# Performance work log

Hardware: AMD Instinct MI355X
Metric: run time of the kernel (lower is better)

Reference implementation:

```python
import jax, jax.numpy as jnp
from jax import lax
import numpy as np

B, C, H, W = 16, 32, 128, 128
R = 8      # region_num
OUT = 32   # out_channels (== in_channels, required by residual add)
K = 3      # kernel_size
PAD = 1    # self.kwargs padding for the correlation conv


def setup_inputs() -> dict:
    key = jax.random.key(0)
    ks = jax.random.split(key, 8)
    n = lambda k, s: jax.random.normal(k, s, dtype=jnp.float32) * 0.05
    return {
        "input": jax.random.normal(ks[0], (B, C, H, W), dtype=jnp.float32),
        "guide_input": jax.random.normal(ks[1], (B, C, H, W), dtype=jnp.float32),
        "w1": n(ks[2], (R * R, C)), "b1": jnp.zeros((R * R,), jnp.float32),
        "w2": n(ks[3], (R, C * OUT, R)), "b2": jnp.zeros((R * C * OUT,), jnp.float32),
        "w_spa": n(ks[4], (R, C)), "b_spa": jnp.zeros((R,), jnp.float32),
        "w_spec": n(ks[5], (R, C)), "b_spec": jnp.zeros((R,), jnp.float32),
        "w_f": n(ks[6], (OUT, 2 * C, 3, 3)), "b_f": jnp.zeros((OUT,), jnp.float32),
    }


def adaptive_avg_pool2d(x, k):
    # torch AdaptiveAvgPool2d bin edges: start=floor(i*H/k), end=ceil((i+1)*H/k)
    Hh, Ww = x.shape[-2], x.shape[-1]
    rows = []
    for i in range(k):
        hs, he = (i * Hh) // k, -(-((i + 1) * Hh) // k)
        cols = []
        for j in range(k):
            ws, we = (j * Ww) // k, -(-((j + 1) * Ww) // k)
            cols.append(x[..., hs:he, ws:we].mean(axis=(-2, -1)))
        rows.append(jnp.stack(cols, axis=-1))
    return jnp.stack(rows, axis=-2)  # [..., k, k]


def asign_index(kernel, guide):
    # kernel: [B, R, OUT, H, W]; guide: [B, R, H, W]
    mask = jax.nn.one_hot(jnp.argmax(guide, axis=1), guide.shape[1], axis=1,
                          dtype=kernel.dtype)  # [B, R, H, W]
    return jnp.sum(kernel * mask[:, :, None], axis=1)  # [B, OUT, H, W]


def reference(input, guide_input, w1, b1, w2, b2, w_spa, b_spa, w_spec, b_spec, w_f, b_f):
    # --- dynamic kernel generation (conv_kernel Sequential) ---
    pooled = adaptive_avg_pool2d(input, K)                                    # [B, C, K, K]
    g = jax.nn.sigmoid(jnp.einsum('bckl,oc->bokl', pooled, w1) + b1[None, :, None, None])  # [B, R*R, K, K]
    g = g.reshape(B, R, R, K, K)
    # grouped 1x1 conv (groups=R): per group in=R, out=C*OUT
    kern = jnp.einsum('brikl,roi->brokl', g, w2).reshape(B, R * C * OUT, K, K)
    kern = kern + b2[None, :, None, None]
    kern = kern.reshape(B, R * OUT, C, K, K)

    # --- correlation: per-sample conv with its own generated kernels (xcorr_fast) ---
    corr = jax.vmap(lambda xi, ki: lax.conv_general_dilated(
        xi[None], ki, (1, 1), [(PAD, PAD), (PAD, PAD)])[0])(input, kern)      # [B, R*OUT, H, W]
    corr = corr.reshape(B, R, OUT, H, W)

    # --- guide features (SpecDynConv / SpecClassifier modeled as 1x1 convs C->R) ---
    gf_spa = jnp.einsum('bchw,rc->brhw', guide_input, w_spa) + b_spa[None, :, None, None]
    gf_spec = jnp.einsum('bchw,rc->brhw', guide_input, w_spec) + b_spec[None, :, None, None]

    # --- argmax one-hot mask select + region-sum ---
    out_spa = asign_index(corr, gf_spa)    # [B, OUT, H, W]
    out_spec = asign_index(corr, gf_spec)  # [B, OUT, H, W]

    # --- fusion conv 3x3 + residual ---
    fused = lax.conv_general_dilated(jnp.concatenate([out_spa, out_spec], axis=1),
                                     w_f, (1, 1), [(1, 1), (1, 1)])
    fused = fused + b_f[None, :, None, None]
    return fused + input
```

## Files before the change

kernel.cpp:

```cpp
#include <hip/hip_runtime.h>
#include <hip/hip_bf16.h>
#include <math.h>

#define Bn 16
#define Cn 32
#define Hn 128
#define Wn 128
#define HW (Hn*Wn)
#define Rn 8
#define OUTn 32
#define PW 130

#define OFF_POOLED 0u
#define OFF_G      18432u
#define OFF_KERNA  55296u
#define OFF_WFA    2414592u
#define OFF_RSEL   2451456u
#define OFF_INTP   3500032u
#define OFF_CATP   20805632u

typedef __attribute__((ext_vector_type(8))) short short8;
typedef __attribute__((ext_vector_type(4))) float floatx4;

static __device__ __forceinline__ unsigned short f2b(float f) {
  __hip_bfloat16 h = __float2bfloat16(f);
  return *reinterpret_cast<unsigned short*>(&h);
}


__global__ void pool_kernel(const float* __restrict__ in, float* __restrict__ pooled) {
  const int bc = blockIdx.x;
  const float* img = in + (size_t)bc * HW;
  __shared__ float red[256];
  const int tid = threadIdx.x;
  const int s0[3] = {0, 42, 85};
  const int e0[3] = {43, 86, 128};
  for (int bi = 0; bi < 3; ++bi) {
    for (int bj = 0; bj < 3; ++bj) {
      const int rs = s0[bi], nr = e0[bi] - rs;
      const int cs = s0[bj], nc = e0[bj] - cs;
      const int n = nr * nc;
      float acc = 0.f;
      for (int i = tid; i < n; i += 256) {
        int y = rs + i / nc, x = cs + i % nc;
        acc += img[y * Wn + x];
      }
      red[tid] = acc; __syncthreads();
      for (int st = 128; st > 0; st >>= 1) {
        if (tid < st) red[tid] += red[tid + st];
        __syncthreads();
      }
      if (tid == 0) pooled[bc * 9 + bi * 3 + bj] = red[0] / (float)n;
      __syncthreads();
    }
  }
}

__global__ void g_kernel(const float* __restrict__ pooled, const float* __restrict__ w1,
                         const float* __restrict__ b1, float* __restrict__ g) {
  const int idx = blockIdx.x * 256 + threadIdx.x;
  if (idx >= Bn * 64 * 9) return;
  const int bin = idx % 9;
  const int o = (idx / 9) % 64;
  const int b = idx / (9 * 64);
  float acc = b1[o];
  #pragma unroll
  for (int c = 0; c < Cn; ++c)
    acc = fmaf(pooled[(b * Cn + c) * 9 + bin], w1[o * Cn + c], acc);
  g[idx] = 1.f / (1.f + expf(-acc));
}

__global__ void kern_kernel(const float* __restrict__ g, const float* __restrict__ w2,
                            const float* __restrict__ b2, short* __restrict__ kernA) {
  const int idx = blockIdx.x * 256 + threadIdx.x;
  if (idx >= Bn * 8 * 9 * 1024) return;
  const int j  = idx & 7;
  const int m  = (idx >> 3) & 15;
  const int kg = (idx >> 7) & 3;
  const int h  = (idx >> 9) & 1;
  const int t  = (idx >> 10) % 9;
  const int br = idx / 9216;
  const int r = br & 7, b = br >> 3;
  const int c = kg * 8 + j;
  const int u = h * 16 + m;
  const int jidx = u * 32 + c;
  float acc = b2[r * 1024 + jidx];
  #pragma unroll
  for (int i = 0; i < 8; ++i)
    acc = fmaf(g[(b * 64 + r * 8 + i) * 9 + t], w2[(r * 1024 + jidx) * 8 + i], acc);
  kernA[idx] = (short)f2b(acc);
}

__global__ void wf_kernel(const float* __restrict__ w_f, short* __restrict__ wfA) {
  int idx = blockIdx.x * 256 + threadIdx.x;
  if (idx >= 18432) return;
  const int j  = idx & 7;
  const int m  = (idx >> 3) & 15;
  const int kg = (idx >> 7) & 3;
  const int h  = (idx >> 9) & 1;
  const int kb = idx >> 10;
  const int tap = kb >> 1, ch = kb & 1;
  const int ci = ch * 32 + kg * 8 + j;
  const int o = h * 16 + m;
  wfA[idx] = (short)f2b(w_f[(o * 64 + ci) * 9 + tap]);
}


__global__ __launch_bounds__(256) void tr_kernel(const float* __restrict__ in,
                                                 uint4* __restrict__ inTp) {
  __shared__ float lds[32][65];
  const int blk = blockIdx.x;
  const int b = blk >> 8;
  const int p0 = (blk & 255) * 64;
  const int tid = threadIdx.x;
  const int pl = tid & 63;
  const int c0 = tid >> 6;
  #pragma unroll
  for (int cc = 0; cc < 8; ++cc) {
    const int c = cc * 4 + c0;
    lds[c][pl] = in[(size_t)(b * 32 + c) * HW + p0 + pl];
  }
  __syncthreads();
  const int pw = tid >> 2;
  const int cg = (tid & 3) * 8;
  unsigned int w0 = (unsigned)f2b(lds[cg + 0][pw]) | ((unsigned)f2b(lds[cg + 1][pw]) << 16);
  unsigned int w1 = (unsigned)f2b(lds[cg + 2][pw]) | ((unsigned)f2b(lds[cg + 3][pw]) << 16);
  unsigned int w2 = (unsigned)f2b(lds[cg + 4][pw]) | ((unsigned)f2b(lds[cg + 5][pw]) << 16);
  unsigned int w3 = (unsigned)f2b(lds[cg + 6][pw]) | ((unsigned)f2b(lds[cg + 7][pw]) << 16);
  const int p = p0 + pw;
  const int y = p >> 7, x = p & 127;
  const size_t pp = (size_t)(b * PW + y + 1) * PW + (x + 1);
  inTp[pp * 4 + (tid & 3)] = make_uint4(w0, w1, w2, w3);
}


__global__ void rsel_kernel(const float* __restrict__ guide,
                            const float* __restrict__ w_spa, const float* __restrict__ b_spa,
                            const float* __restrict__ w_spec, const float* __restrict__ b_spec,
                            int* __restrict__ rsel) {
  const int idx = blockIdx.x * 256 + threadIdx.x;
  const int b = idx >> 14;
  const int p = idx & (HW - 1);
  float gv[Cn];
  const float* gp = guide + (size_t)b * Cn * HW + p;
  #pragma unroll
  for (int c = 0; c < Cn; ++c) gv[c] = gp[c * HW];
  int best1 = 0, best2 = 0;
  float bv1 = -1e30f, bv2 = -1e30f;
  for (int r = 0; r < Rn; ++r) {
    float v1 = b_spa[r], v2 = b_spec[r];
    #pragma unroll
    for (int c = 0; c < Cn; ++c) {
      v1 = fmaf(gv[c], w_spa[r * Cn + c], v1);
      v2 = fmaf(gv[c], w_spec[r * Cn + c], v2);
    }
    if (v1 > bv1) { bv1 = v1; best1 = r; }
    if (v2 > bv2) { bv2 = v2; best2 = r; }
  }
  rsel[idx] = best1 | (best2 << 8);
}


__global__ __launch_bounds__(256) void stageB_kernel(
    const char* __restrict__ inTp, const short* __restrict__ kernA,
    const int* __restrict__ rsel, char* __restrict__ catp) {
  const int id = blockIdx.x;
  const int chunk = id & 7, r = (id >> 3) & 7, b = id >> 6;
  const int pbase = chunk * 2048;
  __shared__ int lcount;
  __shared__ unsigned short list[4096];
  const int tid = threadIdx.x;
  if (tid == 0) lcount = 0;
  __syncthreads();
  const int* rs = rsel + b * HW + pbase;
  for (int i = tid; i < 2048; i += 256) {
    int v = rs[i];
    if ((v & 255) == r) { int k = atomicAdd(&lcount, 1); list[k] = (unsigned short)i; }
    if ((v >> 8) == r)  { int k = atomicAdd(&lcount, 1); list[k] = (unsigned short)(i | 2048); }
  }
  __syncthreads();
  const int cnt = lcount;
  const int lane = tid & 63, wid = tid >> 6;
  const int l15 = lane & 15, kg = lane >> 4;

  short8 aw[18];
  {
    const short* kb = kernA + (size_t)(b * 8 + r) * 18 * 512;
    #pragma unroll
    for (int f = 0; f < 18; ++f)
      aw[f] = *(const short8*)(kb + f * 512 + kg * 128 + l15 * 8);
  }

  for (int g = wid; g * 16 < cnt; g += 4) {
    const int e16 = g * 16 + l15;
    const bool ev = e16 < cnt;
    const int ent = list[ev ? e16 : 0];
    const int p = pbase + (ent & 2047);
    const int which = ent >> 11;
    const int y = p >> 7, x = p & 127;
    const size_t pp = (size_t)(b * PW + y + 1) * PW + (x + 1);
    const char* base = inTp + pp * 64 + kg * 16;
    floatx4 acc0 = {0.f, 0.f, 0.f, 0.f}, acc1 = {0.f, 0.f, 0.f, 0.f};
    #pragma unroll
    for (int t = 0; t < 9; ++t) {
      const int dy = t / 3 - 1, dx = t % 3 - 1;
      const short8 bx = *(const short8*)(base + (dy * PW + dx) * 64);
      acc0 = __builtin_amdgcn_mfma_f32_16x16x32_bf16(aw[t * 2 + 0], bx, acc0, 0, 0, 0);
      acc1 = __builtin_amdgcn_mfma_f32_16x16x32_bf16(aw[t * 2 + 1], bx, acc1, 0, 0, 0);
    }
    if (ev) {
      char* op = catp + pp * 128 + which * 64 + kg * 8;
      uint2 v0, v1;
      v0.x = (unsigned)f2b(acc0[0]) | ((unsigned)f2b(acc0[1]) << 16);
      v0.y = (unsigned)f2b(acc0[2]) | ((unsigned)f2b(acc0[3]) << 16);
      v1.x = (unsigned)f2b(acc1[0]) | ((unsigned)f2b(acc1[1]) << 16);
      v1.y = (unsigned)f2b(acc1[2]) | ((unsigned)f2b(acc1[3]) << 16);
      *(uint2*)op = v0;
      *(uint2*)(op + 32) = v1;
    }
  }
}


__global__ __launch_bounds__(256) void stageC_kernel(
    const char* __restrict__ catp, const short* __restrict__ wfA,
    const float* __restrict__ b_f, const float* __restrict__ in,
    float* __restrict__ out) {
  __shared__ short lwf[18432];
  const int tid = threadIdx.x;
  {
    const uint4* src = (const uint4*)wfA;
    uint4* dst = (uint4*)lwf;
    #pragma unroll
    for (int i = 0; i < 9; ++i)
      dst[i * 256 + tid] = src[i * 256 + tid];
  }
  __syncthreads();
  const int id = blockIdx.x;
  const int b = id >> 6, seg = id & 63;
  const int lane = tid & 63, wid = tid >> 6;
  const int l15 = lane & 15, kg = lane >> 4;
  const int pix = seg * 256 + wid * 64 + l15;

  const char* bq[4];
  #pragma unroll
  for (int q = 0; q < 4; ++q) {
    const int p = pix + q * 16;
    const int y = p >> 7, x = p & 127;
    bq[q] = catp + ((size_t)(b * PW + y + 1) * PW + (x + 1)) * 128 + kg * 16;
  }
  floatx4 acc[2][4] = {};
  #pragma unroll 1
  for (int kb = 0; kb < 18; ++kb) {
    const int tap = kb >> 1, ch = kb & 1;
    const int dy = tap / 3 - 1, dx = tap % 3 - 1;
    const int goff = (dy * PW + dx) * 128 + ch * 64;
    const short8 a0 = *(const short8*)&lwf[(kb * 2 + 0) * 512 + kg * 128 + l15 * 8];
    const short8 a1 = *(const short8*)&lwf[(kb * 2 + 1) * 512 + kg * 128 + l15 * 8];
    #pragma unroll
    for (int q = 0; q < 4; ++q) {
      const short8 bx = *(const short8*)(bq[q] + goff);
      acc[0][q] = __builtin_amdgcn_mfma_f32_16x16x32_bf16(a0, bx, acc[0][q], 0, 0, 0);
      acc[1][q] = __builtin_amdgcn_mfma_f32_16x16x32_bf16(a1, bx, acc[1][q], 0, 0, 0);
    }
  }
  #pragma unroll
  for (int h = 0; h < 2; ++h) {
    const int o0 = h * 16 + kg * 4;
    #pragma unroll
    for (int q = 0; q < 4; ++q) {
      const int p = pix + q * 16;
      #pragma unroll
      for (int reg = 0; reg < 4; ++reg) {
        const size_t oi = (size_t)(b * 32 + o0 + reg) * HW + p;
        out[oi] = acc[h][q][reg] + b_f[o0 + reg] + in[oi];
      }
    }
  }
}


extern "C" void kernel_launch(void* const* d_in, const int* in_sizes, int n_in,
                              void* d_out, int out_size, void* d_ws, size_t ws_size,
                              hipStream_t stream) {
  const float* input  = (const float*)d_in[0];
  const float* guide  = (const float*)d_in[1];
  const float* w1     = (const float*)d_in[2];
  const float* b1     = (const float*)d_in[3];
  const float* w2     = (const float*)d_in[4];
  const float* b2     = (const float*)d_in[5];
  const float* w_spa  = (const float*)d_in[6];
  const float* b_spa  = (const float*)d_in[7];
  const float* w_spec = (const float*)d_in[8];
  const float* b_spec = (const float*)d_in[9];
  const float* w_f    = (const float*)d_in[10];
  const float* b_f    = (const float*)d_in[11];
  float* out = (float*)d_out;

  char* ws = (char*)d_ws;
  float* pooled = (float*)(ws + OFF_POOLED);
  float* g      = (float*)(ws + OFF_G);
  short* kernA  = (short*)(ws + OFF_KERNA);
  short* wfA    = (short*)(ws + OFF_WFA);
  int*   rsel   = (int*)(ws + OFF_RSEL);
  uint4* inTp   = (uint4*)(ws + OFF_INTP);
  char*  catp   = (char*)(ws + OFF_CATP);

  hipMemsetAsync(ws + OFF_INTP, 0, 17305600u + 34611200u, stream);

  pool_kernel<<<Bn * Cn, 256, 0, stream>>>(input, pooled);
  g_kernel<<<(Bn * 64 * 9 + 255) / 256, 256, 0, stream>>>(pooled, w1, b1, g);
  kern_kernel<<<Bn * 8 * 9 * 1024 / 256, 256, 0, stream>>>(g, w2, b2, kernA);
  wf_kernel<<<72, 256, 0, stream>>>(w_f, wfA);
  tr_kernel<<<Bn * 256, 256, 0, stream>>>(input, inTp);
  rsel_kernel<<<Bn * HW / 256, 256, 0, stream>>>(guide, w_spa, b_spa, w_spec, b_spec, rsel);
  stageB_kernel<<<1024, 256, 0, stream>>>((const char*)inTp, kernA, rsel, catp);
  stageC_kernel<<<1024, 256, 0, stream>>>(catp, wfA, b_f, input, out);
}
```

Baseline: 271.5 us.

## Zero only halo borders, parallelize pooling per bin, tune stageC unroll and occupancy

Replaces the 52MB workspace memset with a small kernel that zeroes only the one-pixel halo border of the padded inTp and catp buffers, relying on tr_kernel and stageB to fully write the interiors. The pooling kernel is restructured to one 64-thread block per (b,c,bin) with a wavefront shuffle reduction instead of serial bins and LDS tree reductions. stageC gets a launch-bounds occupancy hint and a partial unroll of its tap loop. The risk is correctness if any interior location was previously relying on the memset.

```diff
diff --git a/kernel.cpp b/kernel.cpp
--- a/kernel.cpp
+++ b/kernel.cpp
@@ -28,32 +28,24 @@
 }
 
 
-__global__ void pool_kernel(const float* __restrict__ in, float* __restrict__ pooled) {
-  const int bc = blockIdx.x;
-  const float* img = in + (size_t)bc * HW;
-  __shared__ float red[256];
-  const int tid = threadIdx.x;
+__global__ __launch_bounds__(64) void pool_kernel(const float* __restrict__ in,
+                                                  float* __restrict__ pooled) {
+  const int blk = blockIdx.x;
+  const int bin = blk % 9, bc = blk / 9;
+  const int bi = bin / 3, bj = bin % 3;
   const int s0[3] = {0, 42, 85};
   const int e0[3] = {43, 86, 128};
-  for (int bi = 0; bi < 3; ++bi) {
-    for (int bj = 0; bj < 3; ++bj) {
-      const int rs = s0[bi], nr = e0[bi] - rs;
-      const int cs = s0[bj], nc = e0[bj] - cs;
-      const int n = nr * nc;
-      float acc = 0.f;
-      for (int i = tid; i < n; i += 256) {
-        int y = rs + i / nc, x = cs + i % nc;
-        acc += img[y * Wn + x];
-      }
-      red[tid] = acc; __syncthreads();
-      for (int st = 128; st > 0; st >>= 1) {
-        if (tid < st) red[tid] += red[tid + st];
-        __syncthreads();
-      }
-      if (tid == 0) pooled[bc * 9 + bi * 3 + bj] = red[0] / (float)n;
-      __syncthreads();
-    }
-  }
+  const int rs = s0[bi], re = e0[bi];
+  const int cs = s0[bj], ce = e0[bj];
+  const int n = (re - rs) * (ce - cs);
+  const float* img = in + (size_t)bc * HW;
+  float acc = 0.f;
+  for (int y = rs; y < re; ++y)
+    for (int x = cs + (int)threadIdx.x; x < ce; x += 64)
+      acc += img[y * Wn + x];
+  #pragma unroll
+  for (int off = 32; off > 0; off >>= 1) acc += __shfl_down(acc, off, 64);
+  if (threadIdx.x == 0) pooled[bc * 9 + bin] = acc / (float)n;
 }
 
 __global__ void g_kernel(const float* __restrict__ pooled, const float* __restrict__ w1,
@@ -103,6 +95,24 @@
   const int ci = ch * 32 + kg * 8 + j;
   const int o = h * 16 + m;
   wfA[idx] = (short)f2b(w_f[(o * 64 + ci) * 9 + tap]);
+}
+
+
+__global__ void halo_kernel(uint4* __restrict__ inTp, uint4* __restrict__ catp) {
+  const int idx = blockIdx.x * 256 + threadIdx.x;
+  if (idx >= Bn * 520) return;
+  const int b = idx / 520, i = idx % 520;
+  int y, x;
+  if (i < 130)      { y = 0;       x = i; }
+  else if (i < 260) { y = 129;     x = i - 130; }
+  else if (i < 390) { y = i - 260; x = 0; }
+  else              { y = i - 390; x = 129; }
+  const size_t pp = (size_t)(b * PW + y) * PW + x;
+  const uint4 z = make_uint4(0u, 0u, 0u, 0u);
+  #pragma unroll
+  for (int q = 0; q < 4; ++q) inTp[pp * 4 + q] = z;
+  #pragma unroll
+  for (int q = 0; q < 8; ++q) catp[pp * 8 + q] = z;
 }
 
 
@@ -222,7 +232,7 @@
 }
 
 
-__global__ __launch_bounds__(256) void stageC_kernel(
+__global__ __launch_bounds__(256, 4) void stageC_kernel(
     const char* __restrict__ catp, const short* __restrict__ wfA,
     const float* __restrict__ b_f, const float* __restrict__ in,
     float* __restrict__ out) {
@@ -250,7 +260,7 @@
     bq[q] = catp + ((size_t)(b * PW + y + 1) * PW + (x + 1)) * 128 + kg * 16;
   }
   floatx4 acc[2][4] = {};
-  #pragma unroll 1
+  #pragma unroll 3
   for (int kb = 0; kb < 18; ++kb) {
     const int tap = kb >> 1, ch = kb & 1;
     const int dy = tap / 3 - 1, dx = tap % 3 - 1;
@@ -306,12 +316,11 @@
   uint4* inTp   = (uint4*)(ws + OFF_INTP);
   char*  catp   = (char*)(ws + OFF_CATP);
 
-  hipMemsetAsync(ws + OFF_INTP, 0, 17305600u + 34611200u, stream);
-
-  pool_kernel<<<Bn * Cn, 256, 0, stream>>>(input, pooled);
+  pool_kernel<<<Bn * Cn * 9, 64, 0, stream>>>(input, pooled);
   g_kernel<<<(Bn * 64 * 9 + 255) / 256, 256, 0, stream>>>(pooled, w1, b1, g);
   kern_kernel<<<Bn * 8 * 9 * 1024 / 256, 256, 0, stream>>>(g, w2, b2, kernA);
   wf_kernel<<<72, 256, 0, stream>>>(w_f, wfA);
+  halo_kernel<<<(Bn * 520 + 255) / 256, 256, 0, stream>>>(inTp, (uint4*)catp);
   tr_kernel<<<Bn * 256, 256, 0, stream>>>(input, inTp);
   rsel_kernel<<<Bn * HW / 256, 256, 0, stream>>>(guide, w_spa, b_spa, w_spec, b_spec, rsel);
   stageB_kernel<<<1024, 256, 0, stream>>>((const char*)inTp, kernA, rsel, catp);
```

New measurement: 252.9 us. -6.9%, faster.
